# Optimization experiments

Measured on AMD Instinct MI355X. Metric: run time of the kernel, lower is better.

## Reference

```python
import jax, jax.numpy as jnp
import numpy as np

P1, P2 = 24, 168          # period1 (daily), period2 (weekly)
MAX_H = 336               # max(hs)
BS, N, F = 64, 512, 16


def mult_seasindex(y, p):
    # average each phase over the first two full cycles, normalize by the mean
    bs, n, f = y.shape
    avg = y[:, :2 * p, :].reshape(bs, 2, p, f).mean(axis=1)          # (bs, p, f)
    return avg / y[:, :2 * p, :].mean(axis=1, keepdims=True)


def mult_init_params(y):
    bs, n, f = y.shape
    I1 = mult_seasindex(y, P1)                                        # (bs, P1, f)
    w1 = mult_seasindex(y, P2) / jnp.tile(I1, (1, P2 // P1, 1))       # (bs, P2, f)
    x = jnp.concatenate([jnp.zeros((bs, 1, f), y.dtype),
                         jnp.diff(y[:, :P2, :], axis=1)], axis=1)
    t = jnp.mean((y[:, :P2, :] - y[:, P2:2 * P2, :]) / P2 + x, axis=1) / 2
    s = jnp.mean(y[:, :2 * P2, :], axis=1) - (P2 + 0.5) * t
    return I1, w1, t, s


def reference(y, alphas, betas, gammas, omegas, phis):
    bs, n, f = y.shape
    a = jax.nn.sigmoid(alphas)
    b = jax.nn.sigmoid(betas)
    g = jax.nn.sigmoid(gammas)
    o = jax.nn.sigmoid(omegas)

    Ic, wc, t, s = mult_init_params(y)

    idx1 = jnp.arange(n) % P1
    idx2 = jnp.arange(n) % P2
    ys = jnp.transpose(y, (1, 0, 2))                                  # (n, bs, f)

    def step(carry, inp):
        Ic, wc, s, t = carry
        yt, i1, i2 = inp
        Icv = jax.lax.dynamic_slice_in_dim(Ic, i1, 1, axis=1)[:, 0, :]
        wcv = jax.lax.dynamic_slice_in_dim(wc, i2, 1, axis=1)[:, 0, :]
        yhat_t = (s + t) * Icv * wcv
        snew = a * (yt / (Icv * wcv)) + (1 - a) * (s + t)
        tnew = b * (snew - s) + (1 - b) * t
        Icn = jax.lax.dynamic_update_slice_in_dim(
            Ic, (g * (yt / (snew * wcv)) + (1 - g) * Icv)[:, None, :], i1, axis=1)
        wcn = jax.lax.dynamic_update_slice_in_dim(
            wc, (o * (yt / (snew * Icv)) + (1 - o) * wcv)[:, None, :], i2, axis=1)
        return (Icn, wcn, snew, tnew), yhat_t

    (Ic, wc, s, t), yhat = jax.lax.scan(step, (Ic, wc, s, t), (ys, idx1, idx2))
    yhat = jnp.transpose(yhat, (1, 0, 2))                             # (bs, n, f)

    Ic = jnp.roll(Ic, (-n) % P1, axis=1)
    wc = jnp.roll(wc, (-n) % P2, axis=1)
    e = y - yhat

    # forecast horizon (multiplicative, enable_ar=False)
    h = jnp.arange(1, MAX_H + 1, dtype=y.dtype)
    ca = s[:, None, :] + h[None, :, None] * t[:, None, :]             # (bs, MAX_H, f)
    cb = jnp.tile(Ic, (1, MAX_H // P1 + 1, 1))[:, :MAX_H, :]
    cc = jnp.tile(wc, (1, MAX_H // P2 + 1, 1))[:, :MAX_H, :]
    fcast = ca * cb * cc
    return fcast, yhat, e, Ic, wc, t, s


def setup_inputs() -> dict:
    key = jax.random.key(0)
    k0, k1, k2, k3, k4, k5 = jax.random.split(key, 6)
    y = jax.random.uniform(k0, (BS, N, F), jnp.float32, minval=5.0, maxval=15.0)
    p = lambda k: 0.001 + 0.01 * jax.random.normal(k, (F,), jnp.float32)
    return {"y": y, "alphas": p(k1), "betas": p(k2), "gammas": p(k3),
            "omegas": p(k4), "phis": p(k5)}
```

## Files before the change

### kernel.cpp

```cpp
#include <hip/hip_runtime.h>
#include <math.h>


#define P1c   24
#define P2c   168
#define NSTEP 512
#define BSc   64
#define NFc   16
#define MAXH  336
#define NT    32
#define NSERIES 1024

#define OFF_FC   0
#define OFF_YH   (BSc * MAXH * NFc)
#define OFF_E    (OFF_YH + BSc * NSTEP * NFc)
#define OFF_IC   (OFF_E  + BSc * NSTEP * NFc)
#define OFF_WC   (OFF_IC + BSc * P1c * NFc)
#define OFF_T    (OFF_WC + BSc * P2c * NFc)
#define OFF_S    (OFF_T  + BSc * NFc)

#define WS_NEED ((size_t)194 * NSERIES * sizeof(double))

__device__ __forceinline__ double nrcp(double a) {
    double x = __builtin_amdgcn_rcp(a);
    x = fma(fma(-a, x, 1.0), x, x);
    x = fma(fma(-a, x, 1.0), x, x);
    return x;
}

__device__ __forceinline__ double nrcp1(double a) {
    double x = __builtin_amdgcn_rcp(a);
    x = fma(fma(-a, x, 1.0), x, x);
    return x;
}

template<int I>
__device__ __forceinline__ double bcast8(double v) {
    constexpr int pat = (I << 5) | 0x18;
    int lo = __builtin_amdgcn_ds_swizzle(__double2loint(v), pat);
    int hi = __builtin_amdgcn_ds_swizzle(__double2hiint(v), pat);
    return __hiloint2double(hi, lo);
}
template<int M>
__device__ __forceinline__ double xor8(double v) {
    constexpr int pat = (M << 10) | 0x1f;
    int lo = __builtin_amdgcn_ds_swizzle(__double2loint(v), pat);
    int hi = __builtin_amdgcn_ds_swizzle(__double2hiint(v), pat);
    return __hiloint2double(hi, lo);
}

__global__ __launch_bounds__(128, 1)
void dshw_scanw(const float* __restrict__ y,
                const float* __restrict__ alphas,
                const float* __restrict__ betas,
                const float* __restrict__ gammas,
                const float* __restrict__ omegas,
                double* __restrict__ wsst,
                float* __restrict__ out)
{
    __shared__ double sW[P2c][NFc];
    __shared__ __align__(16) float sY[NSTEP][NFc];

    const int tid   = threadIdx.x;
    const int s_loc = tid >> 3;
    const int j     = tid & 7;
    const int bb    = blockIdx.x;
    const int f     = s_loc;
    const int g     = bb * NFc + s_loc;

    const float4* __restrict__ y4 =
        (const float4*)(y + (size_t)bb * NSTEP * NFc);
    #pragma unroll 4
    for (int i = tid; i < (NSTEP * NFc) / 4; i += 128) {
        float4 v = y4[i];
        *(float4*)&sY[i >> 2][(i & 3) * 4] = v;
    }
    __syncthreads();

    const double al = 1.0 / (1.0 + exp(-(double)alphas[f]));
    const double be = 1.0 / (1.0 + exp(-(double)betas[f]));
    const double ga = 1.0 / (1.0 + exp(-(double)gammas[f]));
    const double om = 1.0 / (1.0 + exp(-(double)omegas[f]));
    const double one_m_al = 1.0 - al, one_m_be = 1.0 - be;
    const double one_p_be = 1.0 + be;
    const double one_m_ga = 1.0 - ga, one_m_om = 1.0 - om;
    const double inv_al = nrcp(al);
    const double ga_al  = ga * inv_al;
    const double om_al  = om * inv_al;
    const double A_ = one_p_be * one_m_al + one_m_be;

    double Pl = (j == 0) ? 1.0 : 0.0;
    double Ql = 0.0;
    {
        double p = 1.0, q = 0.0, pn = 0.0, qn = 1.0;
        #pragma unroll
        for (int it = 1; it <= 7; ++it) {
            double p2 = fma(A_, p, -pn);
            double q2 = fma(A_, q, -qn);
            pn = one_m_al * p; qn = one_m_al * q;
            p = p2; q = q2;
            if (j == it) { Pl = p; Ql = q; }
        }
    }
    double R_[8];
    R_[0] = one_p_be;
    {
        double r = one_p_be, rn = 1.0;
        #pragma unroll
        for (int m = 1; m < 8; ++m) {
            double r2 = fma(A_, r, -rn);
            rn = one_m_al * r;
            r = r2;
            R_[m] = r;
        }
    }
    double cf[8];
    #pragma unroll
    for (int i = 0; i < 8; ++i) cf[i] = 0.0;
    #pragma unroll
    for (int i = 0; i < 7; ++i) {
        #pragma unroll
        for (int m = 0; m + i + 1 <= 7; ++m) {
            if (j == i + m + 1) cf[i] = R_[m];
        }
    }

    double pa = 0.0, pb = 0.0;
    #pragma unroll
    for (int m = 0; m < 21; ++m) {
        pa += (double)sY[j + 8 * m][s_loc];
        pb += (double)sY[j + 8 * m + P2c][s_loc];
    }
    pa += xor8<1>(pa); pb += xor8<1>(pb);
    pa += xor8<2>(pa); pb += xor8<2>(pb);
    pa += xor8<4>(pa); pb += xor8<4>(pb);
    const double sa = pa, sb = pb;

    double Icr_own[3];
    {
        double icv[3];
        double pc = 0.0;
        #pragma unroll
        for (int m2 = 0; m2 < 3; ++m2) {
            const int ph = j + 8 * m2;
            double v0 = (double)sY[ph][s_loc];
            double v1 = (double)sY[ph + P1c][s_loc];
            icv[m2] = 0.5 * (v0 + v1);
            pc += v0 + v1;
        }
        pc += xor8<1>(pc);
        pc += xor8<2>(pc);
        pc += xor8<4>(pc);
        const double inv_mean48 = 48.0 * nrcp(pc);
        #pragma unroll
        for (int m2 = 0; m2 < 3; ++m2) Icr_own[m2] = icv[m2] * inv_mean48;
    }

    const double mean336     = (sa + sb) * (1.0 / 336.0);
    const double inv_mean336 = nrcp(mean336);
    {
        double rI[3];
        #pragma unroll
        for (int m2 = 0; m2 < 3; ++m2)
            rI[m2] = inv_mean336 * nrcp(Icr_own[m2]);
        #pragma unroll
        for (int m = 0; m < 21; ++m) {
            const int row = j + 8 * m;
            double v0 = (double)sY[row][s_loc];
            double v1 = (double)sY[row + P2c][s_loc];
            sW[row][s_loc] = 0.5 * (v0 + v1) * rI[m % 3];
        }
    }

    double tt0 = 0.5 * ((sa - sb) * (1.0 / (168.0 * 168.0)) +
                        ((double)sY[P2c - 1][s_loc] - (double)sY[0][s_loc]) * (1.0 / 168.0));
    double ss0 = mean336 - 168.5 * tt0;

    double spt0 = ss0 + tt0;
    double snp0 = ss0;

    double xPrev = 0.0, wcPrev = 0.0;
    int wrow = 0, prow = 0, Kb = 0;

#define WIN8(SEL, PSEL, HASD)                                                 \
    {                                                                         \
        double wcv = sW[wrow + j][s_loc];                                     \
        double yv  = (double)sY[Kb + j][s_loc];                               \
        if (HASD) {                                                           \
            Icr_own[PSEL] *= fma(ga_al, xPrev, one_m_ga);                     \
            sW[prow + j][s_loc] = wcPrev * fma(om_al, xPrev, one_m_om);       \
        }                                                                     \
        double iw  = Icr_own[SEL] * wcv;                                      \
        double inv = nrcp1(iw);                                               \
        double aur = (al * yv) * inv;                                         \
        double acc = fma(Pl, spt0, Ql * snp0);                                \
        acc = fma(cf[0], bcast8<0>(aur), acc);                                \
        acc = fma(cf[1], bcast8<1>(aur), acc);                                \
        acc = fma(cf[2], bcast8<2>(aur), acc);                                \
        acc = fma(cf[3], bcast8<3>(aur), acc);                                \
        acc = fma(cf[4], bcast8<4>(aur), acc);                                \
        acc = fma(cf[5], bcast8<5>(aur), acc);                                \
        acc = fma(cf[6], bcast8<6>(aur), acc);                                \
        acc = fma(cf[7], bcast8<7>(aur), acc);                                \
        double s6b = bcast8<6>(acc);                                          \
        double s7b = bcast8<7>(acc);                                          \
        double a6b = bcast8<6>(aur);                                          \
        double a7b = bcast8<7>(aur);                                          \
        double yhat = acc * iw;                                               \
        sY[Kb + j][s_loc] = (float)yhat;                                      \
        double snw = fma(one_m_al, acc, aur);                                 \
        xPrev  = aur * __builtin_amdgcn_rcp(snw);                             \
        wcPrev = wcv;                                                         \
        double snew7 = fma(one_m_al, s7b, a7b);                               \
        double snew6 = fma(one_m_al, s6b, a6b);                               \
        spt0 = fma(one_p_be, snew7, fma(one_m_be, s7b, -snew6));              \
        snp0 = snew7;                                                         \
        prow = wrow;                                                          \
        wrow = (wrow + 8 == P2c) ? 0 : wrow + 8;                              \
        Kb += 8;                                                              \
    }

    WIN8(0, 0, false)
    WIN8(1, 0, true)
    WIN8(2, 1, true)
    for (int k = 0; k < 20; ++k) {
        WIN8(0, 2, true)
        WIN8(1, 0, true)
        WIN8(2, 1, true)
    }
    WIN8(0, 2, true)
#undef WIN8

    Icr_own[0] *= fma(ga_al, xPrev, one_m_ga);
    sW[prow + j][s_loc] = wcPrev * fma(om_al, xPrev, one_m_om);

    const double ss_f = snp0;
    const double tt_f = spt0 - snp0;

    wsst[(size_t)(j     ) * NSERIES + g] = Icr_own[0];
    wsst[(size_t)(j + 8 ) * NSERIES + g] = Icr_own[1];
    wsst[(size_t)(j + 16) * NSERIES + g] = Icr_own[2];
    #pragma unroll
    for (int m = 0; m < 21; ++m) {
        const int row = j + 8 * m;
        wsst[(size_t)(P1c + row) * NSERIES + g] = sW[row][s_loc];
    }
    if (j == 0) {
        wsst[(size_t)192 * NSERIES + g] = ss_f;
        wsst[(size_t)193 * NSERIES + g] = tt_f;
        out[OFF_T + bb * NFc + f] = (float)tt_f;
        out[OFF_S + bb * NFc + f] = (float)ss_f;
    }

    __syncthreads();
    float* __restrict__ yho = out + OFF_YH + (size_t)bb * NSTEP * NFc;
    #pragma unroll 4
    for (int i = tid; i < (NSTEP * NFc) / 4; i += 128) {
        ((float4*)yho)[i] = *(const float4*)&sY[i >> 2][(i & 3) * 4];
    }
}

__global__ __launch_bounds__(256)
void dshw_epilogue(const double* __restrict__ ws,
                   const float* __restrict__ yin,
                   float* __restrict__ out)
{
    const int f      = threadIdx.x & 15;
    const int isub   = threadIdx.x >> 4;
    const int bb     = blockIdx.x & 63;
    const int chunk  = blockIdx.x >> 6;
    const int item   = chunk * 16 + isub;
    const int series = bb * NFc + f;

    if (item < MAXH) {
        const int k = item;
        double cb = ws[(size_t)((k + 8) % P1c) * NSERIES + series];
        double cc = ws[(size_t)(P1c + (k + 8) % P2c) * NSERIES + series];
        double ss = ws[(size_t)192 * NSERIES + series];
        double tt = ws[(size_t)193 * NSERIES + series];
        double ca = ss + (double)(k + 1) * tt;
        out[OFF_FC + (bb * MAXH + k) * NFc + f] = (float)(ca * cb * cc);
    } else if (item < MAXH + P1c) {
        const int j = item - MAXH;
        out[OFF_IC + (bb * P1c + j) * NFc + f] =
            (float)ws[(size_t)((j + 8) % P1c) * NSERIES + series];
    } else if (item < MAXH + P1c + P2c) {
        const int j = item - (MAXH + P1c);
        out[OFF_WC + (bb * P2c + j) * NFc + f] =
            (float)ws[(size_t)(P1c + (j + 8) % P2c) * NSERIES + series];
    } else {
        const int s = item - (MAXH + P1c + P2c);
        const size_t off = ((size_t)bb * NSTEP + s) * NFc + f;
        float yv = yin[off];
        float yh = out[OFF_YH + off];
        out[OFF_E + off] = yv - yh;
    }
}

__global__ __launch_bounds__(NT, 1)
void dshw_fused(const float* __restrict__ y,
                const float* __restrict__ alphas,
                const float* __restrict__ betas,
                const float* __restrict__ gammas,
                const float* __restrict__ omegas,
                float* __restrict__ out)
{
    __shared__ double sIc[P1c][NT];
    __shared__ double sWc[P2c][NT];

    const int tid = threadIdx.x;
    const int g   = blockIdx.x * NT + tid;
    const int bb  = g >> 4;
    const int f   = g & 15;

    const float* __restrict__ yb = y + (size_t)bb * NSTEP * NFc + f;

    const double al = 1.0 / (1.0 + exp(-(double)alphas[f]));
    const double be = 1.0 / (1.0 + exp(-(double)betas[f]));
    const double ga = 1.0 / (1.0 + exp(-(double)gammas[f]));
    const double om = 1.0 / (1.0 + exp(-(double)omegas[f]));

    double sum48 = 0.0;
    #pragma unroll
    for (int ph = 0; ph < P1c; ++ph) {
        double v0 = (double)yb[ph * NFc];
        double v1 = (double)yb[(ph + P1c) * NFc];
        sIc[ph][tid] = 0.5 * (v0 + v1);
        sum48 += v0 + v1;
    }
    const double inv_mean48 = 48.0 / sum48;
    #pragma unroll
    for (int ph = 0; ph < P1c; ++ph) sIc[ph][tid] *= inv_mean48;

    double sum168a = 0.0, sum168b = 0.0;
    for (int i = 0; i < P2c; ++i) {
        double v0 = (double)yb[i * NFc];
        double v1 = (double)yb[(i + P2c) * NFc];
        sWc[i][tid] = 0.5 * (v0 + v1);
        sum168a += v0;
        sum168b += v1;
    }
    const double mean336 = (sum168a + sum168b) * (1.0 / 336.0);
    for (int i = 0; i < P2c; ++i) {
        sWc[i][tid] = (sWc[i][tid] / mean336) / sIc[i % P1c][tid];
    }

    double tt = 0.5 * ((sum168a - sum168b) * (1.0 / (168.0 * 168.0)) +
                       ((double)yb[(P2c - 1) * NFc] - (double)yb[0]) * (1.0 / 168.0));
    double ss = mean336 - 168.5 * tt;

    float* __restrict__ yh_o = out + OFF_YH + (size_t)bb * NSTEP * NFc + f;
    float* __restrict__ e_o  = out + OFF_E  + (size_t)bb * NSTEP * NFc + f;

    int i1 = 0, i2 = 0;
    int i1p = 2, i2p = 2;

    double Icv0 = sIc[0][tid], Icv1 = sIc[1][tid];
    double wcv0 = sWc[0][tid], wcv1 = sWc[1][tid];
    double yt0 = (double)yb[0 * NFc], yt1 = (double)yb[1 * NFc];
    double yt2 = (double)yb[2 * NFc], yt3 = (double)yb[3 * NFc];

    #pragma unroll 4
    for (int step = 0; step < NSTEP; ++step) {
        double Icv2 = sIc[i1p][tid];
        double wcv2 = sWc[i2p][tid];
        int    pidx = step + 4; pidx = (pidx < NSTEP) ? pidx : (NSTEP - 1);
        double yt4  = (double)yb[pidx * NFc];

        double iw     = Icv0 * wcv0;
        double spt    = ss + tt;
        double yhat   = spt * iw;
        double inv_iw = 1.0 / iw;
        double u      = yt0 * inv_iw;
        double snew   = al * u + (1.0 - al) * spt;
        double tnew   = be * (snew - ss) + (1.0 - be) * tt;
        double q      = yt0 / snew;
        double icn    = ga * (q * (inv_iw * Icv0)) + (1.0 - ga) * Icv0;
        double wcn    = om * (q * (inv_iw * wcv0)) + (1.0 - om) * wcv0;

        sIc[i1][tid] = icn;
        sWc[i2][tid] = wcn;
        yh_o[step * NFc] = (float)yhat;
        e_o[step * NFc]  = (float)(yt0 - yhat);

        ss = snew; tt = tnew;
        Icv0 = Icv1; Icv1 = Icv2;
        wcv0 = wcv1; wcv1 = wcv2;
        yt0 = yt1; yt1 = yt2; yt2 = yt3; yt3 = yt4;
        i1  = (i1  + 1 == P1c) ? 0 : i1  + 1;
        i2  = (i2  + 1 == P2c) ? 0 : i2  + 1;
        i1p = (i1p + 1 == P1c) ? 0 : i1p + 1;
        i2p = (i2p + 1 == P2c) ? 0 : i2p + 1;
    }

    float* __restrict__ fc_o = out + OFF_FC + (size_t)bb * MAXH * NFc + f;
    {
        int k1 = 8, k2 = 8;
        for (int k = 0; k < MAXH; ++k) {
            double cb = sIc[k1][tid];
            double cc = sWc[k2][tid];
            double ca = ss + (double)(k + 1) * tt;
            fc_o[k * NFc] = (float)(ca * cb * cc);
            k1 = (k1 + 1 == P1c) ? 0 : k1 + 1;
            k2 = (k2 + 1 == P2c) ? 0 : k2 + 1;
        }
    }
    {
        float* __restrict__ ic_o = out + OFF_IC + (size_t)bb * P1c * NFc + f;
        int k1 = 8;
        #pragma unroll
        for (int j = 0; j < P1c; ++j) {
            ic_o[j * NFc] = (float)sIc[k1][tid];
            k1 = (k1 + 1 == P1c) ? 0 : k1 + 1;
        }
    }
    {
        float* __restrict__ wc_o = out + OFF_WC + (size_t)bb * P2c * NFc + f;
        int k2 = 8;
        for (int j = 0; j < P2c; ++j) {
            wc_o[j * NFc] = (float)sWc[k2][tid];
            k2 = (k2 + 1 == P2c) ? 0 : k2 + 1;
        }
    }

    out[OFF_T + bb * NFc + f] = (float)tt;
    out[OFF_S + bb * NFc + f] = (float)ss;
}

extern "C" void kernel_launch(void* const* d_in, const int* in_sizes, int n_in,
                              void* d_out, int out_size, void* d_ws, size_t ws_size,
                              hipStream_t stream)
{
    const float* y      = (const float*)d_in[0];
    const float* alphas = (const float*)d_in[1];
    const float* betas  = (const float*)d_in[2];
    const float* gammas = (const float*)d_in[3];
    const float* omegas = (const float*)d_in[4];
    float* out = (float*)d_out;

    if (ws_size >= WS_NEED) {
        double* wsst = (double*)d_ws;
        hipLaunchKernelGGL(dshw_scanw, dim3(BSc), dim3(128), 0, stream,
                           y, alphas, betas, gammas, omegas, wsst, out);
        hipLaunchKernelGGL(dshw_epilogue, dim3(65 * BSc), dim3(256), 0, stream,
                           wsst, y, out);
    } else {
        hipLaunchKernelGGL(dshw_fused, dim3(NSERIES / NT), dim3(NT), 0, stream,
                           y, alphas, betas, gammas, omegas, out);
    }
}
```

Before: 84.99 us.

## Fuse epilogue into scan kernel, computing forecast and residuals in-block

Merges the second epilogue kernel into the scan kernel. The forecast, Ic/wc outputs and residual e are now written directly from shared memory and registers instead of going through a double-precision workspace round trip. This removes one kernel launch and the workspace writes and reads. In exchange, the forecast and e work now runs on only 64 blocks instead of thousands of epilogue threads, and the fallback single-kernel path is deleted.

```diff
diff --git a/kernel.cpp b/kernel.cpp
--- a/kernel.cpp
+++ b/kernel.cpp
@@ -8,7 +8,6 @@
 #define BSc   64
 #define NFc   16
 #define MAXH  336
-#define NT    32
 #define NSERIES 1024
 
 #define OFF_FC   0
@@ -19,8 +18,6 @@
 #define OFF_T    (OFF_WC + BSc * P2c * NFc)
 #define OFF_S    (OFF_T  + BSc * NFc)
 
-#define WS_NEED ((size_t)194 * NSERIES * sizeof(double))
-
 __device__ __forceinline__ double nrcp(double a) {
     double x = __builtin_amdgcn_rcp(a);
     x = fma(fma(-a, x, 1.0), x, x);
@@ -50,15 +47,15 @@
 }
 
 __global__ __launch_bounds__(128, 1)
-void dshw_scanw(const float* __restrict__ y,
-                const float* __restrict__ alphas,
-                const float* __restrict__ betas,
-                const float* __restrict__ gammas,
-                const float* __restrict__ omegas,
-                double* __restrict__ wsst,
-                float* __restrict__ out)
+void dshw_one(const float* __restrict__ y,
+              const float* __restrict__ alphas,
+              const float* __restrict__ betas,
+              const float* __restrict__ gammas,
+              const float* __restrict__ omegas,
+              float* __restrict__ out)
 {
     __shared__ double sW[P2c][NFc];
+    __shared__ double sIc[P1c][NFc];
     __shared__ __align__(16) float sY[NSTEP][NFc];
 
     const int tid   = threadIdx.x;
@@ -66,7 +63,6 @@
     const int j     = tid & 7;
     const int bb    = blockIdx.x;
     const int f     = s_loc;
-    const int g     = bb * NFc + s_loc;
 
     const float4* __restrict__ y4 =
         (const float4*)(y + (size_t)bb * NSTEP * NFc);
@@ -237,194 +233,70 @@
     const double ss_f = snp0;
     const double tt_f = spt0 - snp0;
 
-    wsst[(size_t)(j     ) * NSERIES + g] = Icr_own[0];
-    wsst[(size_t)(j + 8 ) * NSERIES + g] = Icr_own[1];
-    wsst[(size_t)(j + 16) * NSERIES + g] = Icr_own[2];
-    #pragma unroll
-    for (int m = 0; m < 21; ++m) {
-        const int row = j + 8 * m;
-        wsst[(size_t)(P1c + row) * NSERIES + g] = sW[row][s_loc];
+    sIc[j     ][s_loc] = Icr_own[0];
+    sIc[j + 8 ][s_loc] = Icr_own[1];
+    sIc[j + 16][s_loc] = Icr_own[2];
+
+    {
+        float* __restrict__ ic_o = out + OFF_IC + (size_t)bb * P1c * NFc + f;
+        ic_o[((j + 16) % P1c) * NFc] = (float)Icr_own[0];
+        ic_o[( j            ) * NFc] = (float)Icr_own[1];
+        ic_o[((j + 8 ) % P1c) * NFc] = (float)Icr_own[2];
+    }
+    {
+        float* __restrict__ wc_o = out + OFF_WC + (size_t)bb * P2c * NFc + f;
+        #pragma unroll
+        for (int m = 0; m < 21; ++m) {
+            const int row = j + 8 * m;
+            const int jj  = (row >= 8) ? (row - 8) : (row + 160);
+            wc_o[jj * NFc] = (float)sW[row][s_loc];
+        }
     }
     if (j == 0) {
-        wsst[(size_t)192 * NSERIES + g] = ss_f;
-        wsst[(size_t)193 * NSERIES + g] = tt_f;
         out[OFF_T + bb * NFc + f] = (float)tt_f;
         out[OFF_S + bb * NFc + f] = (float)ss_f;
     }
 
     __syncthreads();
-    float* __restrict__ yho = out + OFF_YH + (size_t)bb * NSTEP * NFc;
-    #pragma unroll 4
-    for (int i = tid; i < (NSTEP * NFc) / 4; i += 128) {
-        ((float4*)yho)[i] = *(const float4*)&sY[i >> 2][(i & 3) * 4];
-    }
-}
-
-__global__ __launch_bounds__(256)
-void dshw_epilogue(const double* __restrict__ ws,
-                   const float* __restrict__ yin,
-                   float* __restrict__ out)
-{
-    const int f      = threadIdx.x & 15;
-    const int isub   = threadIdx.x >> 4;
-    const int bb     = blockIdx.x & 63;
-    const int chunk  = blockIdx.x >> 6;
-    const int item   = chunk * 16 + isub;
-    const int series = bb * NFc + f;
-
-    if (item < MAXH) {
-        const int k = item;
-        double cb = ws[(size_t)((k + 8) % P1c) * NSERIES + series];
-        double cc = ws[(size_t)(P1c + (k + 8) % P2c) * NSERIES + series];
-        double ss = ws[(size_t)192 * NSERIES + series];
-        double tt = ws[(size_t)193 * NSERIES + series];
-        double ca = ss + (double)(k + 1) * tt;
-        out[OFF_FC + (bb * MAXH + k) * NFc + f] = (float)(ca * cb * cc);
-    } else if (item < MAXH + P1c) {
-        const int j = item - MAXH;
-        out[OFF_IC + (bb * P1c + j) * NFc + f] =
-            (float)ws[(size_t)((j + 8) % P1c) * NSERIES + series];
-    } else if (item < MAXH + P1c + P2c) {
-        const int j = item - (MAXH + P1c);
-        out[OFF_WC + (bb * P2c + j) * NFc + f] =
-            (float)ws[(size_t)(P1c + (j + 8) % P2c) * NSERIES + series];
-    } else {
-        const int s = item - (MAXH + P1c + P2c);
-        const size_t off = ((size_t)bb * NSTEP + s) * NFc + f;
-        float yv = yin[off];
-        float yh = out[OFF_YH + off];
-        out[OFF_E + off] = yv - yh;
-    }
-}
-
-__global__ __launch_bounds__(NT, 1)
-void dshw_fused(const float* __restrict__ y,
-                const float* __restrict__ alphas,
-                const float* __restrict__ betas,
-                const float* __restrict__ gammas,
-                const float* __restrict__ omegas,
-                float* __restrict__ out)
-{
-    __shared__ double sIc[P1c][NT];
-    __shared__ double sWc[P2c][NT];
-
-    const int tid = threadIdx.x;
-    const int g   = blockIdx.x * NT + tid;
-    const int bb  = g >> 4;
-    const int f   = g & 15;
-
-    const float* __restrict__ yb = y + (size_t)bb * NSTEP * NFc + f;
-
-    const double al = 1.0 / (1.0 + exp(-(double)alphas[f]));
-    const double be = 1.0 / (1.0 + exp(-(double)betas[f]));
-    const double ga = 1.0 / (1.0 + exp(-(double)gammas[f]));
-    const double om = 1.0 / (1.0 + exp(-(double)omegas[f]));
-
-    double sum48 = 0.0;
-    #pragma unroll
-    for (int ph = 0; ph < P1c; ++ph) {
-        double v0 = (double)yb[ph * NFc];
-        double v1 = (double)yb[(ph + P1c) * NFc];
-        sIc[ph][tid] = 0.5 * (v0 + v1);
-        sum48 += v0 + v1;
-    }
-    const double inv_mean48 = 48.0 / sum48;
-    #pragma unroll
-    for (int ph = 0; ph < P1c; ++ph) sIc[ph][tid] *= inv_mean48;
-
-    double sum168a = 0.0, sum168b = 0.0;
-    for (int i = 0; i < P2c; ++i) {
-        double v0 = (double)yb[i * NFc];
-        double v1 = (double)yb[(i + P2c) * NFc];
-        sWc[i][tid] = 0.5 * (v0 + v1);
-        sum168a += v0;
-        sum168b += v1;
-    }
-    const double mean336 = (sum168a + sum168b) * (1.0 / 336.0);
-    for (int i = 0; i < P2c; ++i) {
-        sWc[i][tid] = (sWc[i][tid] / mean336) / sIc[i % P1c][tid];
-    }
-
-    double tt = 0.5 * ((sum168a - sum168b) * (1.0 / (168.0 * 168.0)) +
-                       ((double)yb[(P2c - 1) * NFc] - (double)yb[0]) * (1.0 / 168.0));
-    double ss = mean336 - 168.5 * tt;
-
-    float* __restrict__ yh_o = out + OFF_YH + (size_t)bb * NSTEP * NFc + f;
-    float* __restrict__ e_o  = out + OFF_E  + (size_t)bb * NSTEP * NFc + f;
-
-    int i1 = 0, i2 = 0;
-    int i1p = 2, i2p = 2;
-
-    double Icv0 = sIc[0][tid], Icv1 = sIc[1][tid];
-    double wcv0 = sWc[0][tid], wcv1 = sWc[1][tid];
-    double yt0 = (double)yb[0 * NFc], yt1 = (double)yb[1 * NFc];
-    double yt2 = (double)yb[2 * NFc], yt3 = (double)yb[3 * NFc];
-
-    #pragma unroll 4
-    for (int step = 0; step < NSTEP; ++step) {
-        double Icv2 = sIc[i1p][tid];
-        double wcv2 = sWc[i2p][tid];
-        int    pidx = step + 4; pidx = (pidx < NSTEP) ? pidx : (NSTEP - 1);
-        double yt4  = (double)yb[pidx * NFc];
-
-        double iw     = Icv0 * wcv0;
-        double spt    = ss + tt;
-        double yhat   = spt * iw;
-        double inv_iw = 1.0 / iw;
-        double u      = yt0 * inv_iw;
-        double snew   = al * u + (1.0 - al) * spt;
-        double tnew   = be * (snew - ss) + (1.0 - be) * tt;
-        double q      = yt0 / snew;
-        double icn    = ga * (q * (inv_iw * Icv0)) + (1.0 - ga) * Icv0;
-        double wcn    = om * (q * (inv_iw * wcv0)) + (1.0 - om) * wcv0;
-
-        sIc[i1][tid] = icn;
-        sWc[i2][tid] = wcn;
-        yh_o[step * NFc] = (float)yhat;
-        e_o[step * NFc]  = (float)(yt0 - yhat);
-
-        ss = snew; tt = tnew;
-        Icv0 = Icv1; Icv1 = Icv2;
-        wcv0 = wcv1; wcv1 = wcv2;
-        yt0 = yt1; yt1 = yt2; yt2 = yt3; yt3 = yt4;
-        i1  = (i1  + 1 == P1c) ? 0 : i1  + 1;
-        i2  = (i2  + 1 == P2c) ? 0 : i2  + 1;
-        i1p = (i1p + 1 == P1c) ? 0 : i1p + 1;
-        i2p = (i2p + 1 == P2c) ? 0 : i2p + 1;
-    }
-
-    float* __restrict__ fc_o = out + OFF_FC + (size_t)bb * MAXH * NFc + f;
-    {
-        int k1 = 8, k2 = 8;
-        for (int k = 0; k < MAXH; ++k) {
-            double cb = sIc[k1][tid];
-            double cc = sWc[k2][tid];
-            double ca = ss + (double)(k + 1) * tt;
-            fc_o[k * NFc] = (float)(ca * cb * cc);
-            k1 = (k1 + 1 == P1c) ? 0 : k1 + 1;
-            k2 = (k2 + 1 == P2c) ? 0 : k2 + 1;
-        }
-    }
-    {
-        float* __restrict__ ic_o = out + OFF_IC + (size_t)bb * P1c * NFc + f;
-        int k1 = 8;
-        #pragma unroll
-        for (int j = 0; j < P1c; ++j) {
-            ic_o[j * NFc] = (float)sIc[k1][tid];
-            k1 = (k1 + 1 == P1c) ? 0 : k1 + 1;
-        }
-    }
-    {
-        float* __restrict__ wc_o = out + OFF_WC + (size_t)bb * P2c * NFc + f;
-        int k2 = 8;
-        for (int j = 0; j < P2c; ++j) {
-            wc_o[j * NFc] = (float)sWc[k2][tid];
-            k2 = (k2 + 1 == P2c) ? 0 : k2 + 1;
-        }
-    }
-
-    out[OFF_T + bb * NFc + f] = (float)tt;
-    out[OFF_S + bb * NFc + f] = (float)ss;
+    {
+        float* __restrict__ yho = out + OFF_YH + (size_t)bb * NSTEP * NFc;
+        float* __restrict__ eo  = out + OFF_E  + (size_t)bb * NSTEP * NFc;
+        #pragma unroll 4
+        for (int i = tid; i < (NSTEP * NFc) / 4; i += 128) {
+            float4 yh4 = *(const float4*)&sY[i >> 2][(i & 3) * 4];
+            float4 yv4 = y4[i];
+            ((float4*)yho)[i] = yh4;
+            float4 ev;
+            ev.x = yv4.x - yh4.x; ev.y = yv4.y - yh4.y;
+            ev.z = yv4.z - yh4.z; ev.w = yv4.w - yh4.w;
+            ((float4*)eo)[i] = ev;
+        }
+    }
+    __syncthreads();
+
+    {
+        int p1i = j + 8;
+        int p2i = j + 8;
+        #pragma unroll 6
+        for (int m = 0; m < 42; ++m) {
+            const int k = j + 8 * m;
+            double cb = sIc[p1i][s_loc];
+            double cc = sW[p2i][s_loc];
+            double ca = fma((double)(k + 1), tt_f, ss_f);
+            sY[k][s_loc] = (float)(ca * cb * cc);
+            p1i += 8; p1i = (p1i >= P1c) ? (p1i - P1c) : p1i;
+            p2i += 8; p2i = (p2i >= P2c) ? (p2i - P2c) : p2i;
+        }
+    }
+    __syncthreads();
+
+    {
+        float* __restrict__ fco = out + OFF_FC + (size_t)bb * MAXH * NFc;
+        #pragma unroll 4
+        for (int i = tid; i < (MAXH * NFc) / 4; i += 128) {
+            ((float4*)fco)[i] = *(const float4*)&sY[i >> 2][(i & 3) * 4];
+        }
+    }
 }
 
 extern "C" void kernel_launch(void* const* d_in, const int* in_sizes, int n_in,
@@ -438,14 +310,6 @@
     const float* omegas = (const float*)d_in[4];
     float* out = (float*)d_out;
 
-    if (ws_size >= WS_NEED) {
-        double* wsst = (double*)d_ws;
-        hipLaunchKernelGGL(dshw_scanw, dim3(BSc), dim3(128), 0, stream,
-                           y, alphas, betas, gammas, omegas, wsst, out);
-        hipLaunchKernelGGL(dshw_epilogue, dim3(65 * BSc), dim3(256), 0, stream,
-                           wsst, y, out);
-    } else {
-        hipLaunchKernelGGL(dshw_fused, dim3(NSERIES / NT), dim3(NT), 0, stream,
-                           y, alphas, betas, gammas, omegas, out);
-    }
-}
+    hipLaunchKernelGGL(dshw_one, dim3(BSc), dim3(128), 0, stream,
+                       y, alphas, betas, gammas, omegas, out);
+}
```

New measurement: 83.14 us. -2.2%, faster.
